# Kernel optimization log

Hardware: AMD Instinct MI355X
Metric: run time of the kernel (lower is better)

Reference implementation:

```python
import jax, jax.numpy as jnp
import numpy as np

N, E, D, H = 40000, 640000, 128, 8
HD = D // H  # per-head dim = out_dim // num_heads = 16
EPS_LN = 1e-5


def _ln(x, g, b):
    m = jnp.mean(x, axis=-1, keepdims=True)
    v = jnp.var(x, axis=-1, keepdims=True)
    return (x - m) * jax.lax.rsqrt(v + EPS_LN) * g + b


def setup_inputs() -> dict:
    key = jax.random.key(0)
    ks = jax.random.split(key, 32)
    s = 1.0 / np.sqrt(D)
    w = lambda k, shape, sc=s: jax.random.normal(k, shape, jnp.float32) * sc
    return {
        'h': w(ks[0], (N, D), 1.0),
        'e': w(ks[1], (E, D), 1.0),
        'src': jax.random.randint(ks[2], (E,), 0, N),
        'dst': jax.random.randint(ks[3], (E,), 0, N),
        'WQ': w(ks[4], (D, D)), 'WK': w(ks[5], (D, D)), 'WV': w(ks[6], (D, D)),
        'We': w(ks[7], (D, D)),
        'WOh': w(ks[8], (D, D)), 'bOh': jnp.zeros((D,), jnp.float32),
        'WOe': w(ks[9], (D, D)), 'bOe': jnp.zeros((D,), jnp.float32),
        'g1h': jnp.ones((D,), jnp.float32), 'b1h': jnp.zeros((D,), jnp.float32),
        'g1e': jnp.ones((D,), jnp.float32), 'b1e': jnp.zeros((D,), jnp.float32),
        'Wh1': w(ks[10], (D, 2 * D)), 'bh1': jnp.zeros((2 * D,), jnp.float32),
        'Wh2': w(ks[11], (2 * D, D), 1.0 / np.sqrt(2 * D)), 'bh2': jnp.zeros((D,), jnp.float32),
        'We1': w(ks[12], (D, 2 * D)), 'be1': jnp.zeros((2 * D,), jnp.float32),
        'We2': w(ks[13], (2 * D, D), 1.0 / np.sqrt(2 * D)), 'be2': jnp.zeros((D,), jnp.float32),
        'g2h': jnp.ones((D,), jnp.float32), 'b2h': jnp.zeros((D,), jnp.float32),
        'g2e': jnp.ones((D,), jnp.float32), 'b2e': jnp.zeros((D,), jnp.float32),
    }


def reference(h, e, src, dst, WQ, WK, WV, We, WOh, bOh, WOe, bOe,
              g1h, b1h, g1e, b1e, Wh1, bh1, Wh2, bh2, We1, be1, We2, be2,
              g2h, b2h, g2e, b2e):
    n = h.shape[0]
    # --- multi-head attention over graph edges ---
    Q = (h @ WQ).reshape(n, H, HD)
    K = (h @ WK).reshape(n, H, HD)
    V = (h @ WV).reshape(n, H, HD)
    pe = (e @ We).reshape(-1, H, HD)
    # per-edge elementwise score: K[src] * Q[dst] / sqrt(HD) * proj_e
    score = K[src] * Q[dst] * (1.0 / np.sqrt(HD)) * pe          # [E,H,HD]
    e_out = score.reshape(-1, D)                                 # e_out before exp
    sexp = jnp.exp(jnp.clip(jnp.sum(score, -1, keepdims=True), -5.0, 5.0))  # [E,H,1]
    wV = jax.ops.segment_sum(V[src] * sexp, dst, num_segments=n)  # [N,H,HD]
    z = jax.ops.segment_sum(sexp, dst, num_segments=n)             # [N,H,1]
    h_attn = (wV / (z + 1e-6)).reshape(n, D)
    # --- output proj + residual + LN ---
    h1 = _ln(h + h_attn @ WOh + bOh, g1h, b1h)
    e1 = _ln(e + e_out @ WOe + bOe, g1e, b1e)
    # --- FFN + residual + LN ---
    h2 = _ln(h1 + jax.nn.relu(h1 @ Wh1 + bh1) @ Wh2 + bh2, g2h, b2h)
    e2 = _ln(e1 + jax.nn.relu(e1 @ We1 + be1) @ We2 + be2, g2e, b2e)
    return (h2, e2)
```

## Files before the change

kernel.cpp:

```cpp
#include <hip/hip_runtime.h>
#include <hip/hip_bf16.h>


constexpr int N_ = 40000;
constexpr int E_ = 640000;

typedef __attribute__((ext_vector_type(8))) short bf16x8;
typedef __attribute__((ext_vector_type(4))) float f32x4;

__device__ inline short f2bf(float f) {
    union { __hip_bfloat16 b; short s; } u;
    u.b = __float2bfloat16(f);
    return u.s;
}
__device__ inline float bf2f(unsigned short u) {
    union { unsigned u; float f; } v; v.u = ((unsigned)u) << 16; return v.f;
}
__device__ inline unsigned packbf2(float a, float b) {
    return (unsigned)(unsigned short)f2bf(a) |
           ((unsigned)(unsigned short)f2bf(b) << 16);
}

__device__ inline f32x4 mfma16(bf16x8 a, bf16x8 b, f32x4 c) {
    return __builtin_amdgcn_mfma_f32_16x16x32_bf16(a, b, c, 0, 0, 0);
}

__device__ inline float red16(float v) {
    v += __shfl_xor(v, 1);
    v += __shfl_xor(v, 2);
    v += __shfl_xor(v, 4);
    v += __shfl_xor(v, 8);
    return v;
}

template<int KSTEPS, int LDA>
__device__ inline void load_af(const short* sA, int row, int g, bf16x8* af) {
#pragma unroll
    for (int ks = 0; ks < KSTEPS; ++ks)
        af[ks] = *(const bf16x8*)(sA + row * LDA + ks * 32 + g * 8);
}

template<int KSTEPS>
__device__ inline f32x4 gemm_tileF(const bf16x8* af, const short* sW,
                                   int n, int lane, f32x4 acc) {
#pragma unroll
    for (int ks = 0; ks < KSTEPS; ++ks)
        acc = mfma16(af[ks],
                     *(const bf16x8*)(sW + ((n * 4 + ks) * 64 + lane) * 8), acc);
    return acc;
}

template<int NT>
__device__ inline void loadW(const short* __restrict__ Wsrc, int tid,
                             bf16x8* r) {
    constexpr int P = 2048 / NT;
#pragma unroll
    for (int p = 0; p < P; ++p)
        r[p] = *(const bf16x8*)(Wsrc + (tid + p * NT) * 8);
}
template<int NT>
__device__ inline void writeW(short* sW, int tid, const bf16x8* r) {
    constexpr int P = 2048 / NT;
#pragma unroll
    for (int p = 0; p < P; ++p)
        *(bf16x8*)(sW + (tid + p * NT) * 8) = r[p];
}
template<int NT>
__device__ inline void stageWX(const short* __restrict__ Wsrc, short* sW,
                               int tid) {
    bf16x8 t[2048 / NT];
    loadW<NT>(Wsrc, tid, t);
    writeW<NT>(sW, tid, t);
}

__device__ inline void stage64(const float* __restrict__ gsrc, short* sA,
                               int lane, int rowB) {
    int rr = rowB + (lane >> 2);
    int c0 = (lane & 3) * 32;
    const float* gp = gsrc + (size_t)rr * 128 + c0;
    short* dp = sA + rr * 136 + c0;
#pragma unroll
    for (int p = 0; p < 4; ++p) {
        float4 x = *(const float4*)(gp + p * 8);
        float4 y = *(const float4*)(gp + p * 8 + 4);
        bf16x8 v;
        v[0] = f2bf(x.x); v[1] = f2bf(x.y); v[2] = f2bf(x.z); v[3] = f2bf(x.w);
        v[4] = f2bf(y.x); v[5] = f2bf(y.y); v[6] = f2bf(y.z); v[7] = f2bf(y.w);
        *(bf16x8*)(dp + p * 8) = v;
    }
}

__device__ inline void proj_ln(short* sA, const f32x4* eres, const short* sW,
                               const float* __restrict__ bias,
                               const float* __restrict__ gma,
                               const float* __restrict__ beta,
                               int rowB, int c, int g, int lane, f32x4* x1v) {
    bf16x8 af[4];
    load_af<4, 136>(sA, rowB + c, g, af);
    float sx[4] = {0, 0, 0, 0}, sxx[4] = {0, 0, 0, 0};
#pragma unroll
    for (int n = 0; n < 8; ++n) {
        f32x4 a = gemm_tileF<4>(af, sW, n, lane, f32x4{0.f, 0.f, 0.f, 0.f});
        const int col = n * 16 + c;
        float bo = bias[col];
#pragma unroll
        for (int r = 0; r < 4; ++r) {
            float xv = a[r] + bo + eres[n][r];
            a[r] = xv; sx[r] += xv; sxx[r] += xv * xv;
        }
        x1v[n] = a;
    }
    float mean[4], inv[4];
#pragma unroll
    for (int r = 0; r < 4; ++r) {
        float s = red16(sx[r]), s2 = red16(sxx[r]);
        mean[r] = s * 0.0078125f;
        float var = s2 * 0.0078125f - mean[r] * mean[r];
        inv[r] = rsqrtf(var + 1e-5f);
    }
#pragma unroll
    for (int n = 0; n < 8; ++n) {
        const int col = n * 16 + c;
        float gg = gma[col], bb = beta[col];
#pragma unroll
        for (int r = 0; r < 4; ++r) {
            float v1 = (x1v[n][r] - mean[r]) * inv[r] * gg + bb;
            x1v[n][r] = v1;
            sA[(rowB + g * 4 + r) * 136 + col] = f2bf(v1);
        }
    }
}

template<int NT>
__device__ inline void ffn_lnS(short* sA, short* sW,
                               const short* __restrict__ W1t,
                               const float* __restrict__ b1,
                               const short* __restrict__ W2t,
                               const float* __restrict__ b2,
                               const float* __restrict__ gma,
                               const float* __restrict__ beta,
                               int rowB, int c, int g, int lane, int tid,
                               f32x4* x1v, float* __restrict__ outp, int tb) {
    bf16x8 af[4];
    load_af<4, 136>(sA, rowB + c, g, af);
    bf16x8 wreg[2048 / NT];
    loadW<NT>(W1t, tid, wreg);
#pragma unroll
    for (int half = 0; half < 2; ++half) {
        __syncthreads();
        writeW<NT>(sW, tid, wreg);
        loadW<NT>(W2t + half * 16384, tid, wreg);
        __syncthreads();
#pragma unroll
        for (int n2 = 0; n2 < 8; ++n2) {
            f32x4 a3 = gemm_tileF<4>(af, sW, n2, lane,
                                     f32x4{0.f, 0.f, 0.f, 0.f});
            const int col2 = half * 128 + n2 * 16 + c;
            float bb = b1[col2];
#pragma unroll
            for (int r = 0; r < 4; ++r)
                sA[(rowB + g * 4 + r) * 136 + n2 * 16 + c] =
                    f2bf(fmaxf(a3[r] + bb, 0.f));
        }
        bf16x8 a4[4];
        load_af<4, 136>(sA, rowB + c, g, a4);
        __syncthreads();
        writeW<NT>(sW, tid, wreg);
        if (half == 0) loadW<NT>(W1t + 16384, tid, wreg);
        __syncthreads();
#pragma unroll
        for (int n = 0; n < 8; ++n)
            x1v[n] = gemm_tileF<4>(a4, sW, n, lane, x1v[n]);
    }
    float ty[4] = {0, 0, 0, 0}, tyy[4] = {0, 0, 0, 0};
#pragma unroll
    for (int n = 0; n < 8; ++n) {
        const int col = n * 16 + c;
        float bb = b2[col];
#pragma unroll
        for (int r = 0; r < 4; ++r) {
            float xv = x1v[n][r] + bb;
            x1v[n][r] = xv; ty[r] += xv; tyy[r] += xv * xv;
        }
    }
    float mean[4], inv[4];
#pragma unroll
    for (int r = 0; r < 4; ++r) {
        float s = red16(ty[r]), s2 = red16(tyy[r]);
        mean[r] = s * 0.0078125f;
        float var = s2 * 0.0078125f - mean[r] * mean[r];
        inv[r] = rsqrtf(var + 1e-5f);
    }
#pragma unroll
    for (int n = 0; n < 8; ++n) {
        const int col = n * 16 + c;
        float gg = gma[col], bb = beta[col];
#pragma unroll
        for (int r = 0; r < 4; ++r)
            outp[(size_t)(tb + rowB + g * 4 + r) * 128 + col] =
                (x1v[n][r] - mean[r]) * inv[r] * gg + bb;
    }
}

__global__ void prep_weights(
    const float* __restrict__ WQ, const float* __restrict__ WK,
    const float* __restrict__ WV, const float* __restrict__ We,
    const float* __restrict__ WOh, const float* __restrict__ WOe,
    const float* __restrict__ Wh1, const float* __restrict__ Wh2,
    const float* __restrict__ We1, const float* __restrict__ We2,
    short* __restrict__ out) {
    int i = blockIdx.x * 256 + threadIdx.x;
    if (i < 98304) {
        int m = i >> 14, r = i & 16383;
        const float* W = m == 0 ? WQ : m == 1 ? WK : m == 2 ? WV
                        : m == 3 ? We : m == 4 ? WOh : WOe;
        int blk = r >> 9, l = (r >> 3) & 63, j = r & 7;
        int n = blk >> 2, ks = blk & 3;
        int col = n * 16 + (l & 15);
        int k = ks * 32 + (l >> 4) * 8 + j;
        out[i] = f2bf(W[k * 128 + col]);
    } else if (i < 229376) {
        int j2 = i - 98304;
        int m = j2 >> 15, r = j2 & 32767;
        int half = r >> 14, q = r & 16383;
        int blk = q >> 9, l = (q >> 3) & 63, j = q & 7;
        int n = blk >> 2, ks = blk & 3;
        if (m == 0 || m == 2) {
            const float* W = (m == 0) ? Wh1 : We1;
            int col2 = half * 128 + n * 16 + (l & 15);
            int k = ks * 32 + (l >> 4) * 8 + j;
            out[i] = f2bf(W[k * 256 + col2]);
        } else {
            const float* W = (m == 1) ? Wh2 : We2;
            int col = n * 16 + (l & 15);
            int k = half * 128 + ks * 32 + (l >> 4) * 8 + j;
            out[i] = f2bf(W[k * 128 + col]);
        }
    }
}

__global__ void hist_kernel(const int* __restrict__ dst, int* __restrict__ cnt) {
    int i = blockIdx.x * 256 + threadIdx.x;
    if (i < E_) atomicAdd(&cnt[dst[i]], 1);
}

__global__ void __launch_bounds__(1024) scan_kernel(const int* __restrict__ cnt,
                                                    int* __restrict__ off) {
    __shared__ int part[1024];
    int t = threadIdx.x;
    int base = t * 40;
    int s = 0;
    if (base < N_) {
        int end = min(base + 40, N_);
        for (int i = base; i < end; ++i) s += cnt[i];
    }
    part[t] = s;
    __syncthreads();
    for (int d = 1; d < 1024; d <<= 1) {
        int v = (t >= d) ? part[t - d] : 0;
        __syncthreads();
        part[t] += v;
        __syncthreads();
    }
    int prefix = (t == 0) ? 0 : part[t - 1];
    if (base < N_) {
        int end = min(base + 40, N_);
        int run = prefix;
        for (int i = base; i < end; ++i) { off[i] = run; run += cnt[i]; }
    }
    if (t == 1023) off[N_] = part[1023];
}

__global__ void scatter_kernel(const int* __restrict__ src,
                               const int* __restrict__ dst,
                               const int* __restrict__ off,
                               int* __restrict__ cursor,
                               int* __restrict__ slotOf,
                               int* __restrict__ csr_src) {
    int i = blockIdx.x * 256 + threadIdx.x;
    if (i < E_) {
        int d = dst[i];
        int s = off[d] + atomicAdd(&cursor[d], 1);
        slotOf[i] = s;
        csr_src[s] = src[i];
    }
}

__global__ void __launch_bounds__(256) qkv_kernel(
    const float* __restrict__ hsrc, const short* __restrict__ Wt3,
    unsigned short* __restrict__ Qo, unsigned short* __restrict__ Ko,
    unsigned short* __restrict__ Vo) {
    __shared__ __align__(16) short sA[64 * 136];
    __shared__ __align__(16) short sW[128 * 128];
    const int tid = threadIdx.x;
    const int tb = blockIdx.x * 64;
    const int lane = tid & 63, wave = tid >> 6;
    const int c = lane & 15, g = lane >> 4;
    const int rowB = wave * 16;

    stage64(hsrc + (size_t)tb * 128, sA, lane, rowB);
    bf16x8 af[4];
    load_af<4, 136>(sA, rowB + c, g, af);

    unsigned short* outs[3] = {Qo, Ko, Vo};
#pragma unroll
    for (int w = 0; w < 3; ++w) {
        __syncthreads();
        stageWX<256>(Wt3 + w * 16384, sW, tid);
        __syncthreads();
        unsigned short* op = outs[w];
#pragma unroll
        for (int n = 0; n < 8; ++n) {
            f32x4 a = gemm_tileF<4>(af, sW, n, lane, f32x4{0.f, 0.f, 0.f, 0.f});
            const int col = n * 16 + c;
#pragma unroll
            for (int r = 0; r < 4; ++r)
                op[(size_t)(tb + rowB + g * 4 + r) * 128 + col] =
                    (unsigned short)f2bf(a[r]);
        }
    }
}

__global__ void __launch_bounds__(512) edge_kernel(
    const float* __restrict__ e, const int* __restrict__ src,
    const int* __restrict__ dst, const int* __restrict__ slotOf,
    const unsigned short* __restrict__ Qb, const unsigned short* __restrict__ Kb,
    float* __restrict__ sexpS,
    const short* __restrict__ Wet, const short* __restrict__ WOet,
    const short* __restrict__ We1t, const short* __restrict__ We2t,
    const float* __restrict__ bOe,
    const float* __restrict__ g1e, const float* __restrict__ b1e,
    const float* __restrict__ be1, const float* __restrict__ be2,
    const float* __restrict__ g2e, const float* __restrict__ b2e,
    float* __restrict__ e2out) {
    __shared__ __align__(16) short sA[128 * 136];
    __shared__ __align__(16) short sW[128 * 128];
    const int tid = threadIdx.x;
    const int tb = blockIdx.x * 128;
    const int lane = tid & 63, wave = tid >> 6;
    const int c = lane & 15, g = lane >> 4;
    const int rowB = wave * 16;

    stageWX<512>(Wet, sW, tid);
    stage64(e + (size_t)tb * 128, sA, lane, rowB);

    int pre = 0;
    {
        int li = lane & 15;
        if (lane < 16)       pre = src[tb + rowB + li];
        else if (lane < 32)  pre = dst[tb + rowB + li];
        else if (lane < 48)  pre = slotOf[tb + rowB + li];
    }

    f32x4 eres[8];
#pragma unroll
    for (int n = 0; n < 8; ++n)
#pragma unroll
        for (int r = 0; r < 4; ++r)
            eres[n][r] = e[(size_t)(tb + rowB + g * 4 + r) * 128 + n * 16 + c];

    unsigned krg[16], qrg[16];
#pragma unroll
    for (int k = 0; k < 16; ++k) {
        int sI = __shfl(pre, k);
        krg[k] = *(const unsigned*)(Kb + (size_t)sI * 128 + 2 * lane);
    }
#pragma unroll
    for (int k = 0; k < 16; ++k) {
        int dI = __shfl(pre, 16 + k);
        qrg[k] = *(const unsigned*)(Qb + (size_t)dI * 128 + 2 * lane);
    }

    __syncthreads();

    bf16x8 af[4];
    load_af<4, 136>(sA, rowB + c, g, af);
#pragma unroll
    for (int n = 0; n < 8; ++n) {
        f32x4 p = gemm_tileF<4>(af, sW, n, lane, f32x4{0.f, 0.f, 0.f, 0.f});
#pragma unroll
        for (int r = 0; r < 4; ++r)
            sA[(rowB + g * 4 + r) * 136 + n * 16 + c] = f2bf(p[r]);
    }

    const int head = lane >> 3;
#pragma unroll
    for (int i = 0; i < 16; ++i) {
        const int row = rowB + i;
        const int slot = __shfl(pre, 32 + i);
        unsigned kk = krg[i], qq = qrg[i];
        unsigned pp = *(const unsigned*)(sA + row * 136 + 2 * lane);
        float sc0 = bf2f((unsigned short)kk) * bf2f((unsigned short)qq) *
                    0.25f * bf2f((unsigned short)pp);
        float sc1 = bf2f((unsigned short)(kk >> 16)) *
                    bf2f((unsigned short)(qq >> 16)) * 0.25f *
                    bf2f((unsigned short)(pp >> 16));
        *(unsigned*)(sA + row * 136 + 2 * lane) = packbf2(sc0, sc1);
        float s = sc0 + sc1;
        s += __shfl_xor(s, 1);
        s += __shfl_xor(s, 2);
        s += __shfl_xor(s, 4);
        s = fminf(5.f, fmaxf(-5.f, s));
        if ((lane & 7) == 0)
            sexpS[(size_t)slot * 8 + head] = __expf(s);
    }

    __syncthreads();
    stageWX<512>(WOet, sW, tid);
    __syncthreads();

    f32x4 x1v[8];
    proj_ln(sA, eres, sW, bOe, g1e, b1e, rowB, c, g, lane, x1v);
    ffn_lnS<512>(sA, sW, We1t, be1, We2t, be2, g2e, b2e,
                 rowB, c, g, lane, tid, x1v, e2out, tb);
}

__global__ void __launch_bounds__(256) node_kernel(
    const float* __restrict__ h, const unsigned short* __restrict__ Vb,
    const float* __restrict__ sexpS,
    const int* __restrict__ off, const int* __restrict__ csr_src,
    const short* __restrict__ WOht, const short* __restrict__ Wh1t,
    const short* __restrict__ Wh2t,
    const float* __restrict__ bOh,
    const float* __restrict__ g1h, const float* __restrict__ b1h,
    const float* __restrict__ bh1, const float* __restrict__ bh2,
    const float* __restrict__ g2h, const float* __restrict__ b2h,
    float* __restrict__ h2out) {
    __shared__ __align__(16) short sA[64 * 136];
    __shared__ __align__(16) short sW[128 * 128];
    const int tid = threadIdx.x;
    const int tb = blockIdx.x * 64;
    const int lane = tid & 63, wave = tid >> 6;
    const int c = lane & 15, g = lane >> 4;
    const int rowB = wave * 16;
    const int head = lane >> 3;

    stageWX<256>(WOht, sW, tid);

    f32x4 hres[8];
#pragma unroll
    for (int n = 0; n < 8; ++n)
#pragma unroll
        for (int r = 0; r < 4; ++r)
            hres[n][r] = h[(size_t)(tb + rowB + g * 4 + r) * 128 + n * 16 + c];

    int offv = (lane < 17) ? off[tb + rowB + lane] : 0;

    for (int i = 0; i < 16; ++i) {
        const int b0 = __shfl(offv, i), b1 = __shfl(offv, i + 1);
        float a0 = 0.f, a1 = 0.f, zz = 0.f;
        for (int j0 = b0; j0 < b1; j0 += 8) {
            int jj = j0 + (lane & 7);
            int ci = (jj < b1) ? csr_src[jj] : 0;
            unsigned vv[8]; float sv[8];
#pragma unroll
            for (int k = 0; k < 8; ++k) {
                bool ok = (j0 + k) < b1;
                int cs = __shfl(ci, k);
                vv[k] = ok ? *(const unsigned*)(Vb + (size_t)cs * 128 + 2 * lane)
                           : 0u;
                sv[k] = ok ? sexpS[(size_t)(j0 + k) * 8 + head] : 0.f;
            }
#pragma unroll
            for (int k = 0; k < 8; ++k) {
                a0 += bf2f((unsigned short)vv[k]) * sv[k];
                a1 += bf2f((unsigned short)(vv[k] >> 16)) * sv[k];
                zz += sv[k];
            }
        }
        float iz = 1.f / (zz + 1e-6f);
        *(unsigned*)(sA + (rowB + i) * 136 + 2 * lane) = packbf2(a0 * iz, a1 * iz);
    }

    __syncthreads();

    f32x4 x1v[8];
    proj_ln(sA, hres, sW, bOh, g1h, b1h, rowB, c, g, lane, x1v);
    ffn_lnS<256>(sA, sW, Wh1t, bh1, Wh2t, bh2, g2h, b2h,
                 rowB, c, g, lane, tid, x1v, h2out, tb);
}

extern "C" void kernel_launch(void* const* d_in, const int* in_sizes, int n_in,
                              void* d_out, int out_size, void* d_ws,
                              size_t ws_size, hipStream_t stream) {
    const float* h   = (const float*)d_in[0];
    const float* e   = (const float*)d_in[1];
    const int*   src = (const int*)d_in[2];
    const int*   dst = (const int*)d_in[3];
    const float* WQ  = (const float*)d_in[4];
    const float* WK  = (const float*)d_in[5];
    const float* WV  = (const float*)d_in[6];
    const float* We  = (const float*)d_in[7];
    const float* WOh = (const float*)d_in[8];
    const float* bOh = (const float*)d_in[9];
    const float* WOe = (const float*)d_in[10];
    const float* bOe = (const float*)d_in[11];
    const float* g1h = (const float*)d_in[12];
    const float* b1h = (const float*)d_in[13];
    const float* g1e = (const float*)d_in[14];
    const float* b1e = (const float*)d_in[15];
    const float* Wh1 = (const float*)d_in[16];
    const float* bh1 = (const float*)d_in[17];
    const float* Wh2 = (const float*)d_in[18];
    const float* bh2 = (const float*)d_in[19];
    const float* We1 = (const float*)d_in[20];
    const float* be1 = (const float*)d_in[21];
    const float* We2 = (const float*)d_in[22];
    const float* be2 = (const float*)d_in[23];
    const float* g2h = (const float*)d_in[24];
    const float* b2h = (const float*)d_in[25];
    const float* g2e = (const float*)d_in[26];
    const float* b2e = (const float*)d_in[27];

    unsigned short* Qb = (unsigned short*)d_ws;
    unsigned short* Kb = Qb + (size_t)N_ * 128;
    unsigned short* Vb = Kb + (size_t)N_ * 128;
    float* sexpS = (float*)(Vb + (size_t)N_ * 128);
    int* cnt     = (int*)(sexpS + (size_t)E_ * 8);
    int* cursor  = cnt + N_;
    int* off     = cursor + N_;
    int* slotOf  = off + N_ + 16;
    int* csr_src = slotOf + E_;
    short* Wb    = (short*)(csr_src + E_);

    float* h2out = (float*)d_out;
    float* e2out = h2out + (size_t)N_ * 128;

    prep_weights<<<896, 256, 0, stream>>>(WQ, WK, WV, We, WOh, WOe,
                                          Wh1, Wh2, We1, We2, Wb);
    hipMemsetAsync(cnt, 0, 2 * N_ * sizeof(int), stream);
    hist_kernel<<<E_ / 256, 256, 0, stream>>>(dst, cnt);
    scan_kernel<<<1, 1024, 0, stream>>>(cnt, off);
    scatter_kernel<<<E_ / 256, 256, 0, stream>>>(src, dst, off, cursor,
                                                 slotOf, csr_src);
    qkv_kernel<<<N_ / 64, 256, 0, stream>>>(h, Wb, Qb, Kb, Vb);
    edge_kernel<<<E_ / 128, 512, 0, stream>>>(
        e, src, dst, slotOf, Qb, Kb, sexpS,
        Wb + 3 * 16384, Wb + 5 * 16384,
        Wb + 98304 + 2 * 32768, Wb + 98304 + 3 * 32768,
        bOe, g1e, b1e, be1, be2, g2e, b2e, e2out);
    node_kernel<<<N_ / 64, 256, 0, stream>>>(
        h, Vb, sexpS, off, csr_src,
        Wb + 4 * 16384, Wb + 98304, Wb + 98304 + 32768,
        bOh, g1h, b1h, bh1, bh2, g2h, b2h, h2out);
}
```

Baseline: 497.6 us.

## Double-buffer edge weights through registers with 1024-thread blocks; fold score scale into We

The edge kernel now handles 256 edges per block with 1024 threads and keeps two weight buffers in shared memory. Each next weight matrix is prefetched into registers while the current GEMM runs, which hides the global-load latency and removes the extra barrier pairs. The 1/sqrt(HD) factor is folded into the bf16 copy of We during weight prep, and the FFN and LayerNorm are inlined with per-half staging. Shared memory per block grows to roughly 132 KB and register pressure rises, so fewer blocks fit per CU.

Result: slower. 668.8 us (+34.4%).

```diff
diff --git a/kernel.cpp b/kernel.cpp
--- a/kernel.cpp
+++ b/kernel.cpp
@@ -218,7 +218,9 @@
         int n = blk >> 2, ks = blk & 3;
         int col = n * 16 + (l & 15);
         int k = ks * 32 + (l >> 4) * 8 + j;
-        out[i] = f2bf(W[k * 128 + col]);
+        float v = W[k * 128 + col];
+        if (m == 3) v *= 0.25f;
+        out[i] = f2bf(v);
     } else if (i < 229376) {
         int j2 = i - 98304;
         int m = j2 >> 15, r = j2 & 32767;
@@ -321,7 +323,7 @@
     }
 }
 
-__global__ void __launch_bounds__(512) edge_kernel(
+__global__ void __launch_bounds__(1024, 4) edge_kernel(
     const float* __restrict__ e, const int* __restrict__ src,
     const int* __restrict__ dst, const int* __restrict__ slotOf,
     const unsigned short* __restrict__ Qb, const unsigned short* __restrict__ Kb,
@@ -333,16 +335,14 @@
     const float* __restrict__ be1, const float* __restrict__ be2,
     const float* __restrict__ g2e, const float* __restrict__ b2e,
     float* __restrict__ e2out) {
-    __shared__ __align__(16) short sA[128 * 136];
-    __shared__ __align__(16) short sW[128 * 128];
+    __shared__ __align__(16) short sA[256 * 136];
+    __shared__ __align__(16) short sW0[128 * 128];
+    __shared__ __align__(16) short sW1[128 * 128];
     const int tid = threadIdx.x;
-    const int tb = blockIdx.x * 128;
+    const int tb = blockIdx.x * 256;
     const int lane = tid & 63, wave = tid >> 6;
     const int c = lane & 15, g = lane >> 4;
     const int rowB = wave * 16;
-
-    stageWX<512>(Wet, sW, tid);
-    stage64(e + (size_t)tb * 128, sA, lane, rowB);
 
     int pre = 0;
     {
@@ -352,6 +352,10 @@
         else if (lane < 48)  pre = slotOf[tb + rowB + li];
     }
 
+    bf16x8 wreg[2];
+    loadW<1024>(Wet, tid, wreg);
+    stage64(e + (size_t)tb * 128, sA, lane, rowB);
+
     f32x4 eres[8];
 #pragma unroll
     for (int n = 0; n < 8; ++n)
@@ -371,13 +375,16 @@
         qrg[k] = *(const unsigned*)(Qb + (size_t)dI * 128 + 2 * lane);
     }
 
-    __syncthreads();
+    writeW<1024>(sW0, tid, wreg);
+    __syncthreads();
+
+    loadW<1024>(WOet, tid, wreg);
 
     bf16x8 af[4];
     load_af<4, 136>(sA, rowB + c, g, af);
 #pragma unroll
     for (int n = 0; n < 8; ++n) {
-        f32x4 p = gemm_tileF<4>(af, sW, n, lane, f32x4{0.f, 0.f, 0.f, 0.f});
+        f32x4 p = gemm_tileF<4>(af, sW0, n, lane, f32x4{0.f, 0.f, 0.f, 0.f});
 #pragma unroll
         for (int r = 0; r < 4; ++r)
             sA[(rowB + g * 4 + r) * 136 + n * 16 + c] = f2bf(p[r]);
@@ -391,9 +398,9 @@
         unsigned kk = krg[i], qq = qrg[i];
         unsigned pp = *(const unsigned*)(sA + row * 136 + 2 * lane);
         float sc0 = bf2f((unsigned short)kk) * bf2f((unsigned short)qq) *
-                    0.25f * bf2f((unsigned short)pp);
+                    bf2f((unsigned short)pp);
         float sc1 = bf2f((unsigned short)(kk >> 16)) *
-                    bf2f((unsigned short)(qq >> 16)) * 0.25f *
+                    bf2f((unsigned short)(qq >> 16)) *
                     bf2f((unsigned short)(pp >> 16));
         *(unsigned*)(sA + row * 136 + 2 * lane) = packbf2(sc0, sc1);
         float s = sc0 + sc1;
@@ -405,14 +412,85 @@
             sexpS[(size_t)slot * 8 + head] = __expf(s);
     }
 
-    __syncthreads();
-    stageWX<512>(WOet, sW, tid);
-    __syncthreads();
-
+    writeW<1024>(sW1, tid, wreg);
+    __syncthreads();
+
+    loadW<1024>(We1t, tid, wreg);
     f32x4 x1v[8];
-    proj_ln(sA, eres, sW, bOe, g1e, b1e, rowB, c, g, lane, x1v);
-    ffn_lnS<512>(sA, sW, We1t, be1, We2t, be2, g2e, b2e,
-                 rowB, c, g, lane, tid, x1v, e2out, tb);
+    proj_ln(sA, eres, sW1, bOe, g1e, b1e, rowB, c, g, lane, x1v);
+    writeW<1024>(sW0, tid, wreg);
+    __syncthreads();
+
+    bf16x8 af2[4];
+    load_af<4, 136>(sA, rowB + c, g, af2);
+    loadW<1024>(We2t, tid, wreg);
+#pragma unroll
+    for (int n2 = 0; n2 < 8; ++n2) {
+        f32x4 a3 = gemm_tileF<4>(af2, sW0, n2, lane, f32x4{0.f, 0.f, 0.f, 0.f});
+        float bb = be1[n2 * 16 + c];
+#pragma unroll
+        for (int r = 0; r < 4; ++r)
+            sA[(rowB + g * 4 + r) * 136 + n2 * 16 + c] =
+                f2bf(fmaxf(a3[r] + bb, 0.f));
+    }
+    bf16x8 a40[4];
+    load_af<4, 136>(sA, rowB + c, g, a40);
+    writeW<1024>(sW1, tid, wreg);
+    __syncthreads();
+
+    loadW<1024>(We1t + 16384, tid, wreg);
+#pragma unroll
+    for (int n = 0; n < 8; ++n)
+        x1v[n] = gemm_tileF<4>(a40, sW1, n, lane, x1v[n]);
+    writeW<1024>(sW0, tid, wreg);
+    __syncthreads();
+
+    loadW<1024>(We2t + 16384, tid, wreg);
+#pragma unroll
+    for (int n2 = 0; n2 < 8; ++n2) {
+        f32x4 a3 = gemm_tileF<4>(af2, sW0, n2, lane, f32x4{0.f, 0.f, 0.f, 0.f});
+        float bb = be1[128 + n2 * 16 + c];
+#pragma unroll
+        for (int r = 0; r < 4; ++r)
+            sA[(rowB + g * 4 + r) * 136 + n2 * 16 + c] =
+                f2bf(fmaxf(a3[r] + bb, 0.f));
+    }
+    bf16x8 a41[4];
+    load_af<4, 136>(sA, rowB + c, g, a41);
+    writeW<1024>(sW1, tid, wreg);
+    __syncthreads();
+
+#pragma unroll
+    for (int n = 0; n < 8; ++n)
+        x1v[n] = gemm_tileF<4>(a41, sW1, n, lane, x1v[n]);
+
+    float ty[4] = {0, 0, 0, 0}, tyy[4] = {0, 0, 0, 0};
+#pragma unroll
+    for (int n = 0; n < 8; ++n) {
+        float bb = be2[n * 16 + c];
+#pragma unroll
+        for (int r = 0; r < 4; ++r) {
+            float xv = x1v[n][r] + bb;
+            x1v[n][r] = xv; ty[r] += xv; tyy[r] += xv * xv;
+        }
+    }
+    float mean[4], inv[4];
+#pragma unroll
+    for (int r = 0; r < 4; ++r) {
+        float s = red16(ty[r]), s2 = red16(tyy[r]);
+        mean[r] = s * 0.0078125f;
+        float var = s2 * 0.0078125f - mean[r] * mean[r];
+        inv[r] = rsqrtf(var + 1e-5f);
+    }
+#pragma unroll
+    for (int n = 0; n < 8; ++n) {
+        const int col = n * 16 + c;
+        float gg = g2e[col], bb = b2e[col];
+#pragma unroll
+        for (int r = 0; r < 4; ++r)
+            e2out[(size_t)(tb + rowB + g * 4 + r) * 128 + col] =
+                (x1v[n][r] - mean[r]) * inv[r] * gg + bb;
+    }
 }
 
 __global__ void __launch_bounds__(256) node_kernel(
@@ -534,7 +612,7 @@
     scatter_kernel<<<E_ / 256, 256, 0, stream>>>(src, dst, off, cursor,
                                                  slotOf, csr_src);
     qkv_kernel<<<N_ / 64, 256, 0, stream>>>(h, Wb, Qb, Kb, Vb);
-    edge_kernel<<<E_ / 128, 512, 0, stream>>>(
+    edge_kernel<<<E_ / 256, 1024, 0, stream>>>(
         e, src, dst, slotOf, Qb, Kb, sexpS,
         Wb + 3 * 16384, Wb + 5 * 16384,
         Wb + 98304 + 2 * 32768, Wb + 98304 + 3 * 32768,
```
